# Kernel optimization log

Measured on AMD Instinct MI355X. Metric: run time of the kernel, lower is better.

Reference implementation:

```python
import jax, jax.numpy as jnp
import numpy as np

B, S, IN, H, OUT = 4096, 32, 256, 128, 256


def setup_inputs() -> dict:
    key = jax.random.key(0)
    k = jax.random.split(key, 5)
    x = jax.random.normal(k[0], (B, S, IN), dtype=jnp.float32)
    # Stacked per-subband weights: torch nn.Linear computes x @ W.T + b;
    # here we store W already transposed as [S, in, out].
    W1 = jax.random.normal(k[1], (S, IN, H), dtype=jnp.float32) * (1.0 / np.sqrt(IN))
    b1 = jax.random.normal(k[2], (S, H), dtype=jnp.float32) * 0.01
    W2 = jax.random.normal(k[3], (S, H, OUT), dtype=jnp.float32) * (1.0 / np.sqrt(H))
    b2 = jax.random.normal(k[4], (S, OUT), dtype=jnp.float32) * 0.01
    return {"x": x, "W1": W1, "b1": b1, "W2": W2, "b2": b2}


def reference(x, W1, b1, W2, b2):
    # All subbands fused into one batched GEMM + ReLU + batched GEMM.
    # h: [B, S, H]
    h = jax.nn.relu(jnp.einsum('bsi,sih->bsh', x, W1) + b1)
    # out: [B, S, OUT]
    out = jnp.einsum('bsh,sho->bso', h, W2) + b2
    return out
```

## Files before the change

kernel.cpp:

```cpp
#include <hip/hip_runtime.h>
#include <hip/hip_bf16.h>

#define B_   4096
#define S_   32
#define IN_  256
#define H_   128
#define OUT_ 256

typedef __attribute__((ext_vector_type(8))) short bf16x8;
typedef __attribute__((ext_vector_type(4))) float f32x4;
typedef unsigned long long ull;

__device__ __forceinline__ unsigned short f2bf(float f) {
    union { float f; unsigned u; } v; v.f = f;
    unsigned r = v.u + 0x7FFFu + ((v.u >> 16) & 1u);
    return (unsigned short)(r >> 16);
}

__device__ __forceinline__ unsigned cvt_pk(float lo, float hi) {
    unsigned r;
    asm("v_cvt_pk_bf16_f32 %0, %1, %2" : "=v"(r) : "v"(lo), "v"(hi));
    return r;
}

__global__ void transpose_cvt_both(const float* __restrict__ W1,
                                   const float* __restrict__ W2,
                                   unsigned short* __restrict__ w1t,
                                   unsigned short* __restrict__ w2t) {
    __shared__ float tile[32][33];
    int bid = blockIdx.x;
    const float* in; unsigned short* out; int R, C, rel;
    if (bid < 1024) { in = W1; out = w1t; R = IN_; C = H_;  rel = bid; }
    else            { in = W2; out = w2t; R = H_; C = OUT_; rel = bid - 1024; }
    const int tilesR = R >> 5, tilesC = C >> 5;
    const int s   = rel / (tilesR * tilesC);
    const int rem = rel % (tilesR * tilesC);
    const int tr  = rem / tilesC, tc = rem % tilesC;
    const float* ip = in + (size_t)s * R * C;
    unsigned short* op = out + (size_t)s * C * R;
    const int t  = threadIdx.x;
    const int c  = t & 31;
    const int r4 = t >> 5;
#pragma unroll
    for (int i = 0; i < 4; ++i) {
        int r = r4 * 4 + i;
        tile[r][c] = ip[(size_t)(tr * 32 + r) * C + tc * 32 + c];
    }
    __syncthreads();
#pragma unroll
    for (int i = 0; i < 4; ++i) {
        int orow = r4 * 4 + i;
        int ocol = c;
        op[(size_t)(tc * 32 + orow) * R + tr * 32 + ocol] = f2bf(tile[ocol][orow]);
    }
}

__global__ __launch_bounds__(512, 2) void subband_fused_kernel(
        const float* __restrict__ x,
        const unsigned short* __restrict__ w1t,
        const float* __restrict__ b1,
        const unsigned short* __restrict__ w2t,
        const float* __restrict__ b2,
        float* __restrict__ out) {
    __shared__ __align__(16) unsigned char lds[163840];
    unsigned char* w1l = lds;
    unsigned char* w2l = lds + 65536;

    const int bid   = blockIdx.x;
    const int s     = bid & 31;
    const int chunk = bid >> 5;
    const int tid   = threadIdx.x;
    const int w     = tid >> 6;
    const int lane  = tid & 63;
    const int l15   = lane & 15;
    const int l4    = lane >> 4;
    unsigned char* hsl = lds + 131072 + w * 4096;

    const unsigned short* w1s = w1t + (size_t)s * H_ * IN_;
    const unsigned short* w2s = w2t + (size_t)s * OUT_ * H_;
    const int rw = chunk * 512 + w * 64;

    f32x4 v[16];
    {
        const float* xr = x + ((size_t)(rw + l15) * S_ + s) * IN_ + l4 * 8;
#pragma unroll
        for (int kk = 0; kk < 8; ++kk) {
            asm volatile("global_load_dwordx4 %0, %1, off" : "=v"(v[2*kk])   : "v"(xr + kk*32));
            asm volatile("global_load_dwordx4 %0, %1, off" : "=v"(v[2*kk+1]) : "v"(xr + kk*32 + 4));
        }
    }

#pragma unroll
    for (int n = 0; n < 8; ++n) {
        const int h  = n * 16 + (tid >> 5);
        const int cb = (tid & 31) * 16;
        const bf16x8 val = *(const bf16x8*)((const unsigned char*)w1s
                                            + h * 512 + (cb ^ ((h & 7) << 4)));
        *(bf16x8*)(w1l + n * 8192 + tid * 16) = val;
    }
#pragma unroll
    for (int n = 0; n < 8; ++n) {
        const int o  = n * 32 + (tid >> 4);
        const int cb = (tid & 15) * 16;
        const bf16x8 val = *(const bf16x8*)((const unsigned char*)w2s
                                            + o * 256 + (cb ^ ((o & 7) << 4)));
        *(bf16x8*)(w2l + n * 8192 + tid * 16) = val;
    }

    float4 b1v[8];
#pragma unroll
    for (int hf = 0; hf < 8; ++hf)
        b1v[hf] = *(const float4*)(b1 + s * H_ + hf * 16 + l4 * 4);
    float b2v[16];
#pragma unroll
    for (int j = 0; j < 16; ++j)
        b2v[j] = b2[s * OUT_ + (j >> 3) * 128 + (j & 7) * 16 + l15];

    __syncthreads();

#pragma unroll 1
    for (int t = 0; t < 4; ++t) {
        const int r0 = rw + t * 16;

        asm volatile("s_waitcnt vmcnt(0)"
                     : "+v"(v[0]), "+v"(v[1]), "+v"(v[2]), "+v"(v[3]),
                       "+v"(v[4]), "+v"(v[5]), "+v"(v[6]), "+v"(v[7]),
                       "+v"(v[8]), "+v"(v[9]), "+v"(v[10]), "+v"(v[11]),
                       "+v"(v[12]), "+v"(v[13]), "+v"(v[14]), "+v"(v[15])
                     :: "memory");
        __builtin_amdgcn_sched_barrier(0);

        bf16x8 xb[8];
#pragma unroll
        for (int kk = 0; kk < 8; ++kk) {
            union { unsigned u[4]; bf16x8 b; } p;
            p.u[0] = cvt_pk(v[2*kk][0],   v[2*kk][1]);
            p.u[1] = cvt_pk(v[2*kk][2],   v[2*kk][3]);
            p.u[2] = cvt_pk(v[2*kk+1][0], v[2*kk+1][1]);
            p.u[3] = cvt_pk(v[2*kk+1][2], v[2*kk+1][3]);
            xb[kk] = p.b;
        }

        if (t < 3) {
            const float* xr = x + ((size_t)(r0 + 16 + l15) * S_ + s) * IN_ + l4 * 8;
#pragma unroll
            for (int kk = 0; kk < 8; ++kk) {
                asm volatile("global_load_dwordx4 %0, %1, off" : "=v"(v[2*kk])   : "v"(xr + kk*32));
                asm volatile("global_load_dwordx4 %0, %1, off" : "=v"(v[2*kk+1]) : "v"(xr + kk*32 + 4));
            }
        }

        f32x4 acc[8];
#pragma unroll
        for (int hf = 0; hf < 8; ++hf)
#pragma unroll
            for (int i = 0; i < 4; ++i) acc[hf][i] = 0.0f;
#pragma unroll
        for (int kk = 0; kk < 8; ++kk) {
#pragma unroll
            for (int hf = 0; hf < 8; ++hf) {
                const int h = hf * 16 + l15;
                const bf16x8 wf = *(const bf16x8*)(w1l + h * 512
                                   + ((kk * 64 + l4 * 16) ^ ((h & 7) << 4)));
                acc[hf] = __builtin_amdgcn_mfma_f32_16x16x32_bf16(wf, xb[kk], acc[hf], 0, 0, 0);
            }
        }

#pragma unroll
        for (int hf = 0; hf < 8; ++hf) {
            const int h0 = hf * 16 + l4 * 4;
            unsigned p0 = cvt_pk(fmaxf(acc[hf][0] + b1v[hf].x, 0.f),
                                 fmaxf(acc[hf][1] + b1v[hf].y, 0.f));
            unsigned p1 = cvt_pk(fmaxf(acc[hf][2] + b1v[hf].z, 0.f),
                                 fmaxf(acc[hf][3] + b1v[hf].w, 0.f));
            ull p = (ull)p0 | ((ull)p1 << 32);
            *(ull*)(hsl + l15 * 256 + ((h0 * 2) ^ ((l15 & 7) << 4))) = p;
        }
        asm volatile("s_waitcnt lgkmcnt(0)" ::: "memory");
        __builtin_amdgcn_sched_barrier(0);

        bf16x8 pa[4];
#pragma unroll
        for (int kk = 0; kk < 4; ++kk)
            pa[kk] = *(const bf16x8*)(hsl + l15 * 256
                       + ((kk * 64 + l4 * 16) ^ ((l15 & 7) << 4)));

#pragma unroll
        for (int oh = 0; oh < 2; ++oh) {
            f32x4 acc2[8];
#pragma unroll
            for (int of = 0; of < 8; ++of)
#pragma unroll
                for (int i = 0; i < 4; ++i) acc2[of][i] = 0.0f;
#pragma unroll
            for (int kk = 0; kk < 4; ++kk) {
#pragma unroll
                for (int of = 0; of < 8; ++of) {
                    const int o = oh * 128 + of * 16 + l15;
                    const bf16x8 wf = *(const bf16x8*)(w2l + o * 256
                                       + ((kk * 64 + l4 * 16) ^ ((o & 7) << 4)));
                    acc2[of] = __builtin_amdgcn_mfma_f32_16x16x32_bf16(pa[kk], wf, acc2[of], 0, 0, 0);
                }
            }
#pragma unroll
            for (int of = 0; of < 8; ++of)
#pragma unroll
                for (int i = 0; i < 4; ++i) {
                    const int r = r0 + l4 * 4 + i;
                    out[((size_t)r * S_ + s) * OUT_ + oh * 128 + of * 16 + l15]
                        = acc2[of][i] + b2v[oh * 8 + of];
                }
        }
    }
}

extern "C" void kernel_launch(void* const* d_in, const int* in_sizes, int n_in,
                              void* d_out, int out_size, void* d_ws, size_t ws_size,
                              hipStream_t stream) {
    const float* x  = (const float*)d_in[0];
    const float* W1 = (const float*)d_in[1];
    const float* b1 = (const float*)d_in[2];
    const float* W2 = (const float*)d_in[3];
    const float* b2 = (const float*)d_in[4];
    float* out = (float*)d_out;

    unsigned short* w1t = (unsigned short*)d_ws;
    unsigned short* w2t = w1t + (size_t)S_ * H_ * IN_;

    transpose_cvt_both<<<2048, 256, 0, stream>>>(W1, W2, w1t, w2t);
    subband_fused_kernel<<<256, 512, 0, stream>>>(x, w1t, b1, w2t, b2, out);
}
```

Baseline: 81.25 us.

## Pre-pack weights into MFMA fragment order and transpose second GEMM for vector stores

Weights are repacked by two new kernels straight into per-lane MFMA fragment order, so LDS reads become linear 16-byte loads with no XOR swizzle. The second GEMM swaps operand roles (weights as A, hidden as B), which lets each lane write a contiguous float4 of output instead of scalar stores. Biases are staged in LDS and used to initialise the accumulators. The last W2 group stays in registers to fit LDS, and dropping the occupancy hint from launch bounds may change register allocation.

```diff
diff --git a/kernel.cpp b/kernel.cpp
--- a/kernel.cpp
+++ b/kernel.cpp
@@ -16,202 +16,192 @@
     unsigned r = v.u + 0x7FFFu + ((v.u >> 16) & 1u);
     return (unsigned short)(r >> 16);
 }
-
 __device__ __forceinline__ unsigned cvt_pk(float lo, float hi) {
     unsigned r;
     asm("v_cvt_pk_bf16_f32 %0, %1, %2" : "=v"(r) : "v"(lo), "v"(hi));
     return r;
 }
 
-__global__ void transpose_cvt_both(const float* __restrict__ W1,
-                                   const float* __restrict__ W2,
-                                   unsigned short* __restrict__ w1t,
-                                   unsigned short* __restrict__ w2t) {
-    __shared__ float tile[32][33];
-    int bid = blockIdx.x;
-    const float* in; unsigned short* out; int R, C, rel;
-    if (bid < 1024) { in = W1; out = w1t; R = IN_; C = H_;  rel = bid; }
-    else            { in = W2; out = w2t; R = H_; C = OUT_; rel = bid - 1024; }
-    const int tilesR = R >> 5, tilesC = C >> 5;
-    const int s   = rel / (tilesR * tilesC);
-    const int rem = rel % (tilesR * tilesC);
-    const int tr  = rem / tilesC, tc = rem % tilesC;
-    const float* ip = in + (size_t)s * R * C;
-    unsigned short* op = out + (size_t)s * C * R;
-    const int t  = threadIdx.x;
-    const int c  = t & 31;
-    const int r4 = t >> 5;
-#pragma unroll
-    for (int i = 0; i < 4; ++i) {
-        int r = r4 * 4 + i;
-        tile[r][c] = ip[(size_t)(tr * 32 + r) * C + tc * 32 + c];
+__global__ __launch_bounds__(256) void pack_w1(const float* __restrict__ W1,
+                                               unsigned short* __restrict__ w1f) {
+    __shared__ float tile[32][129];
+    const int bid = blockIdx.x, s = bid >> 3, kk = bid & 7;
+    const int t = threadIdx.x;
+#pragma unroll
+    for (int i = 0; i < 16; ++i) {
+        int idx = t + i * 256;
+        int kl = idx >> 7, h = idx & 127;
+        tile[kl][h] = W1[((size_t)s * IN_ + kk * 32 + kl) * H_ + h];
     }
     __syncthreads();
 #pragma unroll
-    for (int i = 0; i < 4; ++i) {
-        int orow = r4 * 4 + i;
-        int ocol = c;
-        op[(size_t)(tc * 32 + orow) * R + tr * 32 + ocol] = f2bf(tile[ocol][orow]);
-    }
-}
-
-__global__ __launch_bounds__(512, 2) void subband_fused_kernel(
+    for (int rep = 0; rep < 2; ++rep) {
+        int idx = t + rep * 256;
+        int hf = idx >> 6, l = idx & 63, l15 = l & 15, l4 = l >> 4;
+        unsigned short o8[8];
+#pragma unroll
+        for (int j = 0; j < 8; ++j) o8[j] = f2bf(tile[l4 * 8 + j][hf * 16 + l15]);
+        *(bf16x8*)(w1f + (((size_t)(s * 8 + kk) * 8 + hf) * 64 + l) * 8) = *(bf16x8*)o8;
+    }
+}
+
+__global__ __launch_bounds__(256) void pack_w2(const float* __restrict__ W2,
+                                               unsigned short* __restrict__ w2f) {
+    __shared__ float tile[32][257];
+    const int bid = blockIdx.x, s = bid >> 2, kkh = bid & 3;
+    const int t = threadIdx.x;
+#pragma unroll
+    for (int i = 0; i < 32; ++i) {
+        int idx = t + i * 256;
+        int kl = idx >> 8, o = idx & 255;
+        tile[kl][o] = W2[((size_t)s * H_ + kkh * 32 + kl) * OUT_ + o];
+    }
+    __syncthreads();
+#pragma unroll
+    for (int rep = 0; rep < 4; ++rep) {
+        int idx = t + rep * 256;
+        int g = idx >> 6, l = idx & 63, l15 = l & 15, l4 = l >> 4;
+        unsigned short o8[8];
+#pragma unroll
+        for (int j = 0; j < 8; ++j) o8[j] = f2bf(tile[l4 * 8 + j][g * 16 + l15]);
+        *(bf16x8*)(w2f + (((size_t)(s * 16 + g) * 4 + kkh) * 64 + l) * 8) = *(bf16x8*)o8;
+    }
+}
+
+__global__ __launch_bounds__(512) void subband_fused_kernel(
         const float* __restrict__ x,
-        const unsigned short* __restrict__ w1t,
+        const unsigned short* __restrict__ w1f,
+        const unsigned short* __restrict__ w2f,
         const float* __restrict__ b1,
-        const unsigned short* __restrict__ w2t,
         const float* __restrict__ b2,
         float* __restrict__ out) {
-    __shared__ __align__(16) unsigned char lds[163840];
+    __shared__ __align__(16) unsigned char lds[161280];
     unsigned char* w1l = lds;
     unsigned char* w2l = lds + 65536;
-
-    const int bid   = blockIdx.x;
-    const int s     = bid & 31;
+    unsigned char* repb = lds + 126976;
+    float* b1l = (float*)(lds + 159744);
+    float* b2l = (float*)(lds + 160256);
+
+    const int bid = blockIdx.x;
+    const int s   = bid & 31;
     const int chunk = bid >> 5;
-    const int tid   = threadIdx.x;
-    const int w     = tid >> 6;
-    const int lane  = tid & 63;
-    const int l15   = lane & 15;
-    const int l4    = lane >> 4;
-    unsigned char* hsl = lds + 131072 + w * 4096;
-
-    const unsigned short* w1s = w1t + (size_t)s * H_ * IN_;
-    const unsigned short* w2s = w2t + (size_t)s * OUT_ * H_;
+    const int tid = threadIdx.x;
+    const int w = tid >> 6, l = tid & 63, l15 = l & 15, l4 = l >> 4;
+    unsigned char* rep = repb + w * 4096;
     const int rw = chunk * 512 + w * 64;
+
+#define LDG(dst, p) asm volatile("global_load_dwordx4 %0, %1, off" : "=v"(dst) : "v"(p))
 
     f32x4 v[16];
     {
         const float* xr = x + ((size_t)(rw + l15) * S_ + s) * IN_ + l4 * 8;
 #pragma unroll
         for (int kk = 0; kk < 8; ++kk) {
-            asm volatile("global_load_dwordx4 %0, %1, off" : "=v"(v[2*kk])   : "v"(xr + kk*32));
-            asm volatile("global_load_dwordx4 %0, %1, off" : "=v"(v[2*kk+1]) : "v"(xr + kk*32 + 4));
-        }
-    }
-
-#pragma unroll
-    for (int n = 0; n < 8; ++n) {
-        const int h  = n * 16 + (tid >> 5);
-        const int cb = (tid & 31) * 16;
-        const bf16x8 val = *(const bf16x8*)((const unsigned char*)w1s
-                                            + h * 512 + (cb ^ ((h & 7) << 4)));
-        *(bf16x8*)(w1l + n * 8192 + tid * 16) = val;
-    }
-#pragma unroll
-    for (int n = 0; n < 8; ++n) {
-        const int o  = n * 32 + (tid >> 4);
-        const int cb = (tid & 15) * 16;
-        const bf16x8 val = *(const bf16x8*)((const unsigned char*)w2s
-                                            + o * 256 + (cb ^ ((o & 7) << 4)));
-        *(bf16x8*)(w2l + n * 8192 + tid * 16) = val;
-    }
-
-    float4 b1v[8];
-#pragma unroll
-    for (int hf = 0; hf < 8; ++hf)
-        b1v[hf] = *(const float4*)(b1 + s * H_ + hf * 16 + l4 * 4);
-    float b2v[16];
-#pragma unroll
-    for (int j = 0; j < 16; ++j)
-        b2v[j] = b2[s * OUT_ + (j >> 3) * 128 + (j & 7) * 16 + l15];
+            LDG(v[2 * kk],     xr + kk * 32);
+            LDG(v[2 * kk + 1], xr + kk * 32 + 4);
+        }
+    }
+
+    const unsigned char* w1src = (const unsigned char*)(w1f + (size_t)s * 32768);
+#pragma unroll
+    for (int i = 0; i < 8; ++i)
+        *(bf16x8*)(w1l + tid * 16 + i * 8192) = *(const bf16x8*)(w1src + tid * 16 + i * 8192);
+    const unsigned char* w2src = (const unsigned char*)(w2f + (size_t)s * 32768);
+#pragma unroll
+    for (int i = 0; i < 7; ++i)
+        *(bf16x8*)(w2l + tid * 16 + i * 8192) = *(const bf16x8*)(w2src + tid * 16 + i * 8192);
+    if (tid < 256)
+        *(bf16x8*)(w2l + tid * 16 + 57344) = *(const bf16x8*)(w2src + tid * 16 + 57344);
+
+    bf16x8 w2r[4];
+#pragma unroll
+    for (int kkh = 0; kkh < 4; ++kkh)
+        w2r[kkh] = *(const bf16x8*)(w2src + (((size_t)15 * 4 + kkh) * 64 + l) * 16);
+
+    if (tid < 128)      b1l[tid]       = b1[s * H_ + tid];
+    else if (tid < 384) b2l[tid - 128] = b2[s * OUT_ + (tid - 128)];
 
     __syncthreads();
+
+    float* opbase = out + ((size_t)(rw + l15) * S_ + s) * OUT_;
 
 #pragma unroll 1
     for (int t = 0; t < 4; ++t) {
-        const int r0 = rw + t * 16;
-
         asm volatile("s_waitcnt vmcnt(0)"
-                     : "+v"(v[0]), "+v"(v[1]), "+v"(v[2]), "+v"(v[3]),
-                       "+v"(v[4]), "+v"(v[5]), "+v"(v[6]), "+v"(v[7]),
-                       "+v"(v[8]), "+v"(v[9]), "+v"(v[10]), "+v"(v[11]),
-                       "+v"(v[12]), "+v"(v[13]), "+v"(v[14]), "+v"(v[15])
-                     :: "memory");
+            : "+v"(v[0]), "+v"(v[1]), "+v"(v[2]), "+v"(v[3]),
+              "+v"(v[4]), "+v"(v[5]), "+v"(v[6]), "+v"(v[7]),
+              "+v"(v[8]), "+v"(v[9]), "+v"(v[10]), "+v"(v[11]),
+              "+v"(v[12]), "+v"(v[13]), "+v"(v[14]), "+v"(v[15]) :: "memory");
         __builtin_amdgcn_sched_barrier(0);
 
         bf16x8 xb[8];
 #pragma unroll
         for (int kk = 0; kk < 8; ++kk) {
             union { unsigned u[4]; bf16x8 b; } p;
-            p.u[0] = cvt_pk(v[2*kk][0],   v[2*kk][1]);
-            p.u[1] = cvt_pk(v[2*kk][2],   v[2*kk][3]);
-            p.u[2] = cvt_pk(v[2*kk+1][0], v[2*kk+1][1]);
-            p.u[3] = cvt_pk(v[2*kk+1][2], v[2*kk+1][3]);
+            p.u[0] = cvt_pk(v[2 * kk][0],     v[2 * kk][1]);
+            p.u[1] = cvt_pk(v[2 * kk][2],     v[2 * kk][3]);
+            p.u[2] = cvt_pk(v[2 * kk + 1][0], v[2 * kk + 1][1]);
+            p.u[3] = cvt_pk(v[2 * kk + 1][2], v[2 * kk + 1][3]);
             xb[kk] = p.b;
         }
 
         if (t < 3) {
-            const float* xr = x + ((size_t)(r0 + 16 + l15) * S_ + s) * IN_ + l4 * 8;
+            const float* xr = x + ((size_t)(rw + (t + 1) * 16 + l15) * S_ + s) * IN_ + l4 * 8;
 #pragma unroll
             for (int kk = 0; kk < 8; ++kk) {
-                asm volatile("global_load_dwordx4 %0, %1, off" : "=v"(v[2*kk])   : "v"(xr + kk*32));
-                asm volatile("global_load_dwordx4 %0, %1, off" : "=v"(v[2*kk+1]) : "v"(xr + kk*32 + 4));
+                LDG(v[2 * kk],     xr + kk * 32);
+                LDG(v[2 * kk + 1], xr + kk * 32 + 4);
             }
         }
 
-        f32x4 acc[8];
-#pragma unroll
-        for (int hf = 0; hf < 8; ++hf)
-#pragma unroll
-            for (int i = 0; i < 4; ++i) acc[hf][i] = 0.0f;
-#pragma unroll
-        for (int kk = 0; kk < 8; ++kk) {
+        f32x4 acc1[8];
+#pragma unroll
+        for (int hf = 0; hf < 8; ++hf) {
+            const float4 bv = *(const float4*)(b1l + hf * 16 + l4 * 4);
+            acc1[hf][0] = bv.x; acc1[hf][1] = bv.y; acc1[hf][2] = bv.z; acc1[hf][3] = bv.w;
+        }
+#pragma unroll
+        for (int kk = 0; kk < 8; ++kk)
 #pragma unroll
             for (int hf = 0; hf < 8; ++hf) {
-                const int h = hf * 16 + l15;
-                const bf16x8 wf = *(const bf16x8*)(w1l + h * 512
-                                   + ((kk * 64 + l4 * 16) ^ ((h & 7) << 4)));
-                acc[hf] = __builtin_amdgcn_mfma_f32_16x16x32_bf16(wf, xb[kk], acc[hf], 0, 0, 0);
+                const bf16x8 wf = *(const bf16x8*)(w1l + ((kk * 8 + hf) * 64 + l) * 16);
+                acc1[hf] = __builtin_amdgcn_mfma_f32_16x16x32_bf16(wf, xb[kk], acc1[hf], 0, 0, 0);
             }
-        }
 
 #pragma unroll
         for (int hf = 0; hf < 8; ++hf) {
-            const int h0 = hf * 16 + l4 * 4;
-            unsigned p0 = cvt_pk(fmaxf(acc[hf][0] + b1v[hf].x, 0.f),
-                                 fmaxf(acc[hf][1] + b1v[hf].y, 0.f));
-            unsigned p1 = cvt_pk(fmaxf(acc[hf][2] + b1v[hf].z, 0.f),
-                                 fmaxf(acc[hf][3] + b1v[hf].w, 0.f));
+            unsigned p0 = cvt_pk(fmaxf(acc1[hf][0], 0.f), fmaxf(acc1[hf][1], 0.f));
+            unsigned p1 = cvt_pk(fmaxf(acc1[hf][2], 0.f), fmaxf(acc1[hf][3], 0.f));
             ull p = (ull)p0 | ((ull)p1 << 32);
-            *(ull*)(hsl + l15 * 256 + ((h0 * 2) ^ ((l15 & 7) << 4))) = p;
+            const int kkh = hf >> 1;
+            const int l4p = ((hf & 1) << 1) | (l4 >> 1);
+            *(ull*)(rep + kkh * 1024 + (l4p * 16 + l15) * 16 + ((l4 & 1) * 8)) = p;
         }
         asm volatile("s_waitcnt lgkmcnt(0)" ::: "memory");
         __builtin_amdgcn_sched_barrier(0);
 
-        bf16x8 pa[4];
-#pragma unroll
-        for (int kk = 0; kk < 4; ++kk)
-            pa[kk] = *(const bf16x8*)(hsl + l15 * 256
-                       + ((kk * 64 + l4 * 16) ^ ((l15 & 7) << 4)));
-
-#pragma unroll
-        for (int oh = 0; oh < 2; ++oh) {
-            f32x4 acc2[8];
-#pragma unroll
-            for (int of = 0; of < 8; ++of)
-#pragma unroll
-                for (int i = 0; i < 4; ++i) acc2[of][i] = 0.0f;
-#pragma unroll
-            for (int kk = 0; kk < 4; ++kk) {
-#pragma unroll
-                for (int of = 0; of < 8; ++of) {
-                    const int o = oh * 128 + of * 16 + l15;
-                    const bf16x8 wf = *(const bf16x8*)(w2l + o * 256
-                                       + ((kk * 64 + l4 * 16) ^ ((o & 7) << 4)));
-                    acc2[of] = __builtin_amdgcn_mfma_f32_16x16x32_bf16(pa[kk], wf, acc2[of], 0, 0, 0);
-                }
+        bf16x8 hfr[4];
+#pragma unroll
+        for (int kkh = 0; kkh < 4; ++kkh)
+            hfr[kkh] = *(const bf16x8*)(rep + kkh * 1024 + l * 16);
+
+        float* op = opbase + (size_t)t * 16 * S_ * OUT_;
+#pragma unroll
+        for (int g = 0; g < 16; ++g) {
+            const float4 bv = *(const float4*)(b2l + g * 16 + l4 * 4);
+            f32x4 acc2;
+            acc2[0] = bv.x; acc2[1] = bv.y; acc2[2] = bv.z; acc2[3] = bv.w;
+#pragma unroll
+            for (int kkh = 0; kkh < 4; ++kkh) {
+                const bf16x8 wf = (g < 15)
+                    ? *(const bf16x8*)(w2l + ((g * 4 + kkh) * 64 + l) * 16)
+                    : w2r[kkh];
+                acc2 = __builtin_amdgcn_mfma_f32_16x16x32_bf16(wf, hfr[kkh], acc2, 0, 0, 0);
             }
-#pragma unroll
-            for (int of = 0; of < 8; ++of)
-#pragma unroll
-                for (int i = 0; i < 4; ++i) {
-                    const int r = r0 + l4 * 4 + i;
-                    out[((size_t)r * S_ + s) * OUT_ + oh * 128 + of * 16 + l15]
-                        = acc2[of][i] + b2v[oh * 8 + of];
-                }
-        }
-    }
+            *(f32x4*)(op + g * 16 + l4 * 4) = acc2;
+        }
+    }
+#undef LDG
 }
 
 extern "C" void kernel_launch(void* const* d_in, const int* in_sizes, int n_in,
@@ -224,9 +214,10 @@
     const float* b2 = (const float*)d_in[4];
     float* out = (float*)d_out;
 
-    unsigned short* w1t = (unsigned short*)d_ws;
-    unsigned short* w2t = w1t + (size_t)S_ * H_ * IN_;
-
-    transpose_cvt_both<<<2048, 256, 0, stream>>>(W1, W2, w1t, w2t);
-    subband_fused_kernel<<<256, 512, 0, stream>>>(x, w1t, b1, w2t, b2, out);
-}
+    unsigned short* w1f = (unsigned short*)d_ws;
+    unsigned short* w2f = w1f + (size_t)S_ * 8 * 8 * 64 * 8;
+
+    pack_w1<<<S_ * 8, 256, 0, stream>>>(W1, w1f);
+    pack_w2<<<S_ * 4, 256, 0, stream>>>(W2, w2f);
+    subband_fused_kernel<<<256, 512, 0, stream>>>(x, w1f, w2f, b1, b2, out);
+}
```

After: 79.13 us. 2.6% less time.
